# Kernel optimization log

Measured on AMD Instinct MI355X. Metric: run time of the kernel, lower is better.

Reference implementation:

```python
import math
import jax, jax.numpy as jnp
import numpy as np

B, NH, T, N, D = 4, 8, 2048, 256, 512
THETA = 2 ** 16
LN_EPS = 1e-5
RETRIEVAL_SCALE = 1.0
TWO_PI = 2.0 * math.pi


def _freqs(n):
    # get_freqs: 1/theta**(floor(i/2)*2 / n) / (2*pi)
    i = jnp.arange(n, dtype=jnp.float32)
    q = jnp.floor(i / 2.0) * 2.0
    return 1.0 / (THETA ** (q / n)) / TWO_PI


def _rope(phases, v):
    # phases: [1,1,T,N]; v: [B,nh,T,N]
    ph = (phases % 1.0) * TWO_PI
    pc, ps = jnp.cos(ph), jnp.sin(ph)
    ve, vo = v[..., ::2], v[..., 1::2]
    v_rot = jnp.stack((-vo, ve), axis=-1).reshape(v.shape)  # interleaved rotate
    return v * pc + v_rot * ps


def _l2norm(x):
    return x / jnp.maximum(jnp.linalg.norm(x, axis=-1, keepdims=True), 1e-12)


def setup_inputs() -> dict:
    key = jax.random.key(0)
    ks = jax.random.split(key, 8)
    return {
        "Q": jax.random.normal(ks[0], (B, NH, T, N), jnp.float32),
        "V": jax.random.normal(ks[1], (B, NH, T, D), jnp.float32),
        "x_raw": jax.random.normal(ks[2], (B, T, D), jnp.float32),
        "x_next": jax.random.normal(ks[3], (B, T, D), jnp.float32),
        "theta_Q_w": 0.02 * jax.random.normal(ks[4], (N, D), jnp.float32),
        "theta_K_w": 0.02 * jax.random.normal(ks[5], (N, D), jnp.float32),
        "beta_w": 0.02 * jax.random.normal(ks[6], (NH, D), jnp.float32),
        "memory_gate": jnp.full((1, NH, 1, 1), -2.0, jnp.float32),
        "M0": 0.02 * jax.random.normal(ks[7], (B, NH, N, D), jnp.float32),
    }


def _forward(Q, V, x_raw, x_next, theta_Q_w, theta_K_w, beta_w, memory_gate, M0):
    Bq, nh, Tq, Nq = Q.shape
    # ---- causal RoPE linear attention (K is Q; strictly lower-triangular, no softmax)
    freqs = _freqs(Nq)  # [N]
    phases = jnp.arange(Tq, dtype=jnp.float32)[None, None, :, None] * freqs[None, None, None, :]
    QR = _rope(phases, Q)
    scores = jnp.einsum('bhtn,bhsn->bhts', QR, QR)
    mask = jnp.tril(jnp.ones((Tq, Tq), bool), -1)  # diagonal=-1
    scores = jnp.where(mask, scores, 0.0)
    y_standard = scores @ V  # [B,nh,T,D]

    # ---- memory retrieval (position-invariant query)
    Qm = _l2norm(x_raw @ theta_Q_w.T)  # [B,T,N], shared across heads
    y_memory = jnp.einsum('btn,bhnd->bhtd', Qm, M0)
    mu = y_memory.mean(-1, keepdims=True)
    var = y_memory.var(-1, keepdims=True)  # biased, like torch LayerNorm
    y_memory = (y_memory - mu) * jax.lax.rsqrt(var + LN_EPS) * RETRIEVAL_SCALE

    # ---- delta-rule memory update (detached in the original)
    Km = _l2norm(jax.lax.stop_gradient(x_raw @ theta_K_w.T))         # [B,T,N]
    beta = jax.nn.sigmoid(jax.lax.stop_gradient(x_raw @ beta_w.T))   # [B,T,nh]
    Vm = jax.lax.stop_gradient(x_next)                               # [B,T,D]
    M_init = jax.lax.stop_gradient(M0)

    def step(M, inp):
        k, v, b = inp  # k:[B,N] shared across heads, v:[B,D], b:[B,nh]
        v_old = jnp.einsum('bn,bhnd->bhd', k, M)
        v_new = b[..., None] * v[:, None, :] + (1.0 - b[..., None]) * v_old
        M = M + jnp.einsum('bn,bhd->bhnd', k, v_new - v_old)
        return M, None

    M_new, _ = jax.lax.scan(
        step, M_init,
        (jnp.swapaxes(Km, 0, 1), jnp.swapaxes(Vm, 0, 1), jnp.swapaxes(beta, 0, 1)))

    gate = jax.nn.sigmoid(memory_gate)  # [1,nh,1,1]
    y = (1.0 - gate) * y_standard + gate * y_memory
    return y, M_new


def reference(Q, V, x_raw, x_next, theta_Q_w, theta_K_w, beta_w, memory_gate, M0):
    return _forward(Q, V, x_raw, x_next, theta_Q_w, theta_K_w, beta_w, memory_gate, M0)
```

## Files before the change

kernel.cpp:

```cpp
#include <hip/hip_runtime.h>
#include <hip/hip_bf16.h>
#include <math.h>

#define BBATCH 4
#define NHEAD  8
#define TSEQ   2048
#define NDIM   256
#define DDIM   512

typedef float f32x4 __attribute__((ext_vector_type(4)));
typedef short bf16x8 __attribute__((ext_vector_type(8)));

typedef __attribute__((address_space(3))) unsigned int lds_uint;
typedef __attribute__((address_space(1))) unsigned int g_uint;

__device__ __forceinline__ unsigned short f2bf(float f) {
  __hip_bfloat16 h = __float2bfloat16(f);
  return *reinterpret_cast<unsigned short*>(&h);
}
__device__ __forceinline__ float bf2f(unsigned short u) {
  __hip_bfloat16 h;
  *reinterpret_cast<unsigned short*>(&h) = u;
  return __bfloat162float(h);
}
__device__ __forceinline__ f32x4 mfma16(bf16x8 a, bf16x8 b, f32x4 c) {
  return __builtin_amdgcn_mfma_f32_16x16x32_bf16(a, b, c, 0, 0, 0);
}

#define KSW(t) (((((t) & 7) ^ (((t) >> 3) & 3))) << 4)

__global__ __launch_bounds__(256) void rope_kernel(const float* __restrict__ Q,
                                                   unsigned short* __restrict__ QR) {
  long idx = (long)blockIdx.x * 256 + threadIdx.x;
  int pair = (int)(idx & 127);
  long row = idx >> 7;
  int t = (int)(row & (TSEQ - 1));
  float2 q = reinterpret_cast<const float2*>(Q)[idx];
  float freq = exp2f(-(float)pair * 0.125f) * 0.15915494309189535f;
  float phase = (float)t * freq;
  float ph = (phase - floorf(phase)) * 6.283185307179586f;
  float s, c;
  sincosf(ph, &s, &c);
  float o0 = q.x * c - q.y * s;
  float o1 = q.y * c + q.x * s;
  unsigned int pk = (unsigned int)f2bf(o0) | ((unsigned int)f2bf(o1) << 16);
  reinterpret_cast<unsigned int*>(QR)[idx] = pk;
}

__global__ __launch_bounds__(256) void transpose_cast_kernel(
    const float* __restrict__ in, unsigned short* __restrict__ out, int R, int C) {
  __shared__ float tile[64][65];
  long mat = blockIdx.z;
  const float* src = in + mat * (long)R * C;
  unsigned short* dst = out + mat * (long)R * C;
  int c0 = blockIdx.x * 64, r0 = blockIdx.y * 64;
  int tr = threadIdx.x >> 4;
  int tc = (threadIdx.x & 15) * 4;
#pragma unroll
  for (int p = 0; p < 4; ++p) {
    int r = tr + p * 16;
    float4 v = *reinterpret_cast<const float4*>(&src[(long)(r0 + r) * C + c0 + tc]);
    tile[r][tc + 0] = v.x; tile[r][tc + 1] = v.y;
    tile[r][tc + 2] = v.z; tile[r][tc + 3] = v.w;
  }
  __syncthreads();
#pragma unroll
  for (int p = 0; p < 4; ++p) {
    int c = tr + p * 16;
    ushort4 o;
    o.x = f2bf(tile[tc + 0][c]);
    o.y = f2bf(tile[tc + 1][c]);
    o.z = f2bf(tile[tc + 2][c]);
    o.w = f2bf(tile[tc + 3][c]);
    *reinterpret_cast<ushort4*>(&dst[(long)(c0 + c) * R + r0 + tc]) = o;
  }
}

__global__ __launch_bounds__(512) void qkm_kernel(
    const float* __restrict__ x,
    const float* __restrict__ wq,
    const float* __restrict__ wk,
    unsigned short* __restrict__ Qm,
    float* __restrict__ Km) {
  const bool isK = (blockIdx.y == 1);
  const float* w = isK ? wk : wq;
  int r0 = blockIdx.x * 64;
  int wave = threadIdx.x >> 6, lane = threadIdx.x & 63;
  int wm = wave >> 2, wn = wave & 3;
  int khi = lane >> 4, l16 = lane & 15;
  __shared__ unsigned short Ahi[64 * 32], Alo[64 * 32];
  __shared__ unsigned short Bhi[256 * 32], Blo[256 * 32];
  __shared__ float red[4][64];
  f32x4 acc[2][4] = {};
  for (int k0 = 0; k0 < 512; k0 += 32) {
    {
      int row = threadIdx.x >> 3;
      int kc = (threadIdx.x & 7) * 4;
      float4 v = *reinterpret_cast<const float4*>(&x[(long)(r0 + row) * 512 + k0 + kc]);
      float vv[4] = {v.x, v.y, v.z, v.w};
      unsigned int hx[2], lx[2];
      unsigned short h0 = f2bf(vv[0]), h1 = f2bf(vv[1]), h2 = f2bf(vv[2]), h3 = f2bf(vv[3]);
      hx[0] = (unsigned)h0 | ((unsigned)h1 << 16);
      hx[1] = (unsigned)h2 | ((unsigned)h3 << 16);
      lx[0] = (unsigned)f2bf(vv[0] - bf2f(h0)) | ((unsigned)f2bf(vv[1] - bf2f(h1)) << 16);
      lx[1] = (unsigned)f2bf(vv[2] - bf2f(h2)) | ((unsigned)f2bf(vv[3] - bf2f(h3)) << 16);
      int byt = row * 64 + ((kc * 2) ^ ((row & 3) << 4));
      *reinterpret_cast<uint2*>((char*)Ahi + byt) = make_uint2(hx[0], hx[1]);
      *reinterpret_cast<uint2*>((char*)Alo + byt) = make_uint2(lx[0], lx[1]);
    }
#pragma unroll
    for (int p = 0; p < 4; ++p) {
      int idx2 = threadIdx.x + p * 512;
      int row = idx2 >> 3;
      int kc = (idx2 & 7) * 4;
      float4 v = *reinterpret_cast<const float4*>(&w[(long)row * 512 + k0 + kc]);
      float vv[4] = {v.x, v.y, v.z, v.w};
      unsigned short h0 = f2bf(vv[0]), h1 = f2bf(vv[1]), h2 = f2bf(vv[2]), h3 = f2bf(vv[3]);
      unsigned int hx0 = (unsigned)h0 | ((unsigned)h1 << 16);
      unsigned int hx1 = (unsigned)h2 | ((unsigned)h3 << 16);
      unsigned int lx0 = (unsigned)f2bf(vv[0] - bf2f(h0)) | ((unsigned)f2bf(vv[1] - bf2f(h1)) << 16);
      unsigned int lx1 = (unsigned)f2bf(vv[2] - bf2f(h2)) | ((unsigned)f2bf(vv[3] - bf2f(h3)) << 16);
      int byt = row * 64 + ((kc * 2) ^ ((row & 3) << 4));
      *reinterpret_cast<uint2*>((char*)Bhi + byt) = make_uint2(hx0, hx1);
      *reinterpret_cast<uint2*>((char*)Blo + byt) = make_uint2(lx0, lx1);
    }
    __syncthreads();
    bf16x8 ah[2], al[2], bh[4], bl[4];
#pragma unroll
    for (int mi = 0; mi < 2; ++mi) {
      int row = wm * 32 + mi * 16 + l16;
      int byt = row * 64 + ((khi * 16) ^ ((row & 3) << 4));
      ah[mi] = *reinterpret_cast<const bf16x8*>((const char*)Ahi + byt);
      al[mi] = *reinterpret_cast<const bf16x8*>((const char*)Alo + byt);
    }
#pragma unroll
    for (int ni = 0; ni < 4; ++ni) {
      int row = wn * 64 + ni * 16 + l16;
      int byt = row * 64 + ((khi * 16) ^ ((row & 3) << 4));
      bh[ni] = *reinterpret_cast<const bf16x8*>((const char*)Bhi + byt);
      bl[ni] = *reinterpret_cast<const bf16x8*>((const char*)Blo + byt);
    }
#pragma unroll
    for (int mi = 0; mi < 2; ++mi)
#pragma unroll
      for (int ni = 0; ni < 4; ++ni) {
        acc[mi][ni] = mfma16(ah[mi], bh[ni], acc[mi][ni]);
        acc[mi][ni] = mfma16(ah[mi], bl[ni], acc[mi][ni]);
        acc[mi][ni] = mfma16(al[mi], bh[ni], acc[mi][ni]);
      }
    __syncthreads();
  }
  float part[2][4];
#pragma unroll
  for (int mi = 0; mi < 2; ++mi)
#pragma unroll
    for (int r = 0; r < 4; ++r) {
      float s = 0.f;
#pragma unroll
      for (int ni = 0; ni < 4; ++ni) s += acc[mi][ni][r] * acc[mi][ni][r];
      part[mi][r] = s;
    }
#pragma unroll
  for (int off = 1; off < 16; off <<= 1)
#pragma unroll
    for (int mi = 0; mi < 2; ++mi)
#pragma unroll
      for (int r = 0; r < 4; ++r) part[mi][r] += __shfl_xor(part[mi][r], off);
  if (l16 == 0) {
#pragma unroll
    for (int mi = 0; mi < 2; ++mi)
#pragma unroll
      for (int r = 0; r < 4; ++r)
        red[wn][wm * 32 + mi * 16 + khi * 4 + r] = part[mi][r];
  }
  __syncthreads();
#pragma unroll
  for (int mi = 0; mi < 2; ++mi)
#pragma unroll
    for (int r = 0; r < 4; ++r) {
      int row = wm * 32 + mi * 16 + khi * 4 + r;
      float ss = red[0][row] + red[1][row] + red[2][row] + red[3][row];
      float scale = 1.f / fmaxf(sqrtf(ss), 1e-12f);
#pragma unroll
      for (int ni = 0; ni < 4; ++ni) {
        int col = wn * 64 + ni * 16 + l16;
        float val = acc[mi][ni][r] * scale;
        if (isK) Km[(long)(r0 + row) * 256 + col] = val;
        else     Qm[(long)(r0 + row) * 256 + col] = f2bf(val);
      }
    }
}

__global__ __launch_bounds__(64) void beta_kernel(const float* __restrict__ x,
                                                  const float* __restrict__ bw,
                                                  float* __restrict__ beta) {
  long row = blockIdx.x;
  int lane = threadIdx.x;
  const float* xr = x + row * 512;
  float xv[8];
#pragma unroll
  for (int j = 0; j < 8; ++j) xv[j] = xr[lane + j * 64];
#pragma unroll
  for (int hh = 0; hh < 8; ++hh) {
    const float* wr = bw + hh * 512;
    float p = 0.f;
#pragma unroll
    for (int j = 0; j < 8; ++j) p += xv[j] * wr[lane + j * 64];
#pragma unroll
    for (int off = 32; off > 0; off >>= 1) p += __shfl_down(p, off);
    if (lane == 0) beta[row * 8 + hh] = 1.f / (1.f + expf(-p));
  }
}

__global__ __launch_bounds__(256) void wprep_kernel(
    const float* __restrict__ Km, const float* __restrict__ beta,
    unsigned short* __restrict__ Whi, unsigned short* __restrict__ Wlo) {
  __shared__ unsigned short Khi[64 * 256];
  __shared__ unsigned short Klo[64 * 256];
  __shared__ float Bm[64 * 64];
  __shared__ float X[64 * 64];
  __shared__ float bv[64];
  int blk = blockIdx.x, ch = blk & 31, bh = blk >> 5;
  int b = bh >> 3, h = bh & 7;
  int t0 = ch * 64;
  int tid = threadIdx.x, wave = tid >> 6, lane = tid & 63;
  int khi = lane >> 4, l16 = lane & 15;
  {
    int t = tid >> 2, n0 = (tid & 3) * 64;
    const float* kp = Km + ((long)(b * TSEQ) + t0 + t) * 256 + n0;
    char* ph = (char*)Khi + t * 512;
    char* pl = (char*)Klo + t * 512;
#pragma unroll
    for (int i = 0; i < 64; i += 8) {
      float4 v0 = *(const float4*)(kp + i);
      float4 v1 = *(const float4*)(kp + i + 4);
      float vv[8] = {v0.x, v0.y, v0.z, v0.w, v1.x, v1.y, v1.z, v1.w};
      unsigned int hw[4], lw[4];
#pragma unroll
      for (int q = 0; q < 4; ++q) {
        unsigned short h0 = f2bf(vv[2 * q]), h1 = f2bf(vv[2 * q + 1]);
        hw[q] = (unsigned)h0 | ((unsigned)h1 << 16);
        lw[q] = (unsigned)f2bf(vv[2 * q] - bf2f(h0)) |
                ((unsigned)f2bf(vv[2 * q + 1] - bf2f(h1)) << 16);
      }
      int off = ((n0 + i) * 2) ^ ((t & 7) << 4);
      *(uint4*)(ph + off) = make_uint4(hw[0], hw[1], hw[2], hw[3]);
      *(uint4*)(pl + off) = make_uint4(lw[0], lw[1], lw[2], lw[3]);
    }
  }
  if (tid < 64) bv[tid] = beta[((long)(b * TSEQ) + t0 + tid) * 8 + h];
  __syncthreads();
  f32x4 sacc[4] = {};
#pragma unroll
  for (int ks = 0; ks < 8; ++ks) {
    int arow = wave * 16 + l16;
    int koff = (ks * 32 + khi * 8) * 2;
    bf16x8 ah = *(const bf16x8*)((const char*)Khi + arow * 512 + (koff ^ ((arow & 7) << 4)));
    bf16x8 al = *(const bf16x8*)((const char*)Klo + arow * 512 + (koff ^ ((arow & 7) << 4)));
    bf16x8 bhf[4], blf[4];
#pragma unroll
    for (int si = 0; si < 4; ++si) {
      int brow = si * 16 + l16;
      bhf[si] = *(const bf16x8*)((const char*)Khi + brow * 512 + (koff ^ ((brow & 7) << 4)));
      blf[si] = *(const bf16x8*)((const char*)Klo + brow * 512 + (koff ^ ((brow & 7) << 4)));
    }
#pragma unroll
    for (int si = 0; si < 4; ++si) sacc[si] = mfma16(ah, bhf[si], sacc[si]);
#pragma unroll
    for (int si = 0; si < 4; ++si) sacc[si] = mfma16(ah, blf[si], sacc[si]);
#pragma unroll
    for (int si = 0; si < 4; ++si) sacc[si] = mfma16(al, bhf[si], sacc[si]);
  }
#pragma unroll
  for (int si = 0; si < 4; ++si)
#pragma unroll
    for (int r = 0; r < 4; ++r) {
      int t = wave * 16 + khi * 4 + r, s = si * 16 + l16;
      Bm[t * 64 + s] = (s < t) ? bv[t] * sacc[si][r] : 0.f;
    }
  __syncthreads();
  if (wave == 0) {
    for (int t = 0; t < 64; ++t) {
      float xv = (lane == t) ? 1.f : 0.f;
      for (int r = 0; r < t; ++r)
        xv = fmaf(-Bm[t * 64 + r], X[r * 64 + lane], xv);
      X[t * 64 + lane] = xv;
    }
  }
  __syncthreads();
  long base = (long)blk * 4096;
  for (int i = tid; i < 4096; i += 256) {
    int s = i & 63;
    float wv = X[i] * bv[s];
    unsigned short hi = f2bf(wv);
    Whi[base + i] = hi;
    Wlo[base + i] = f2bf(wv - bf2f(hi));
  }
}

__global__ __launch_bounds__(256) void cscan_kernel(
    const float* __restrict__ Km, const float* __restrict__ xn,
    const float* __restrict__ M0,
    const unsigned short* __restrict__ Whi, const unsigned short* __restrict__ Wlo,
    float* __restrict__ Mout) {
  __shared__ unsigned short Mthi[64 * 256];
  __shared__ unsigned short Mtlo[64 * 256];
  __shared__ unsigned short Kr[64 * 256];
  __shared__ unsigned short Wh[64 * 64];
  __shared__ unsigned short Wl[64 * 64];
  __shared__ unsigned short RU0[64 * 64];
  __shared__ unsigned short RU1[64 * 64];
  int blk = blockIdx.x, dsl = blk & 7, bh = blk >> 3;
  int b = bh >> 3;
  int d0 = dsl * 64;
  int tid = threadIdx.x, wave = tid >> 6, lane = tid & 63;
  int khi = lane >> 4, l16 = lane & 15;

  f32x4 macc[4][4];
  const float* M0p = M0 + (long)bh * 256 * 512;
#pragma unroll
  for (int ni = 0; ni < 4; ++ni)
#pragma unroll
    for (int di = 0; di < 4; ++di)
#pragma unroll
      for (int r = 0; r < 4; ++r) {
        int n = wave * 64 + ni * 16 + khi * 4 + r;
        macc[ni][di][r] = M0p[(long)n * 512 + d0 + di * 16 + l16];
      }

#pragma unroll
  for (int ni = 0; ni < 4; ++ni)
#pragma unroll
    for (int di = 0; di < 4; ++di) {
      int n = wave * 64 + ni * 16 + khi * 4;
      int d = di * 16 + l16;
      unsigned short hq[4], lq[4];
#pragma unroll
      for (int r = 0; r < 4; ++r) {
        float v = macc[ni][di][r];
        hq[r] = f2bf(v); lq[r] = f2bf(v - bf2f(hq[r]));
      }
      int off = d * 512 + (((n * 2) ^ ((d & 7) << 4)));
      *(uint2*)((char*)Mthi + off) =
          make_uint2((unsigned)hq[0] | ((unsigned)hq[1] << 16),
                     (unsigned)hq[2] | ((unsigned)hq[3] << 16));
      *(uint2*)((char*)Mtlo + off) =
          make_uint2((unsigned)lq[0] | ((unsigned)lq[1] << 16),
                     (unsigned)lq[2] | ((unsigned)lq[3] << 16));
    }
  __syncthreads();

  for (int ch = 0; ch < 32; ++ch) {
    int tc0 = ch * 64;
    {
      int t = tid >> 2, n0q = (tid & 3) * 64;
      const float* kp = Km + ((long)(b * TSEQ) + tc0 + t) * 256 + n0q;
      char* ph = (char*)Kr + t * 512;
#pragma unroll
      for (int i = 0; i < 64; i += 8) {
        float4 v0 = *(const float4*)(kp + i);
        float4 v1 = *(const float4*)(kp + i + 4);
        unsigned int hw[4];
        hw[0] = (unsigned)f2bf(v0.x) | ((unsigned)f2bf(v0.y) << 16);
        hw[1] = (unsigned)f2bf(v0.z) | ((unsigned)f2bf(v0.w) << 16);
        hw[2] = (unsigned)f2bf(v1.x) | ((unsigned)f2bf(v1.y) << 16);
        hw[3] = (unsigned)f2bf(v1.z) | ((unsigned)f2bf(v1.w) << 16);
        int off = ((n0q + i) * 2) ^ KSW(t);
        *(uint4*)(ph + off) = make_uint4(hw[0], hw[1], hw[2], hw[3]);
      }
    }
    {
      long wbase = ((long)bh * 32 + ch) * 4096;
      int i = tid * 16;
      int t = i >> 6, s = i & 63;
      int o1 = t * 128 + (((s * 2) ^ ((t & 7) << 4)));
      int o2 = t * 128 + ((((s + 8) * 2) ^ ((t & 7) << 4)));
      *(uint4*)((char*)Wh + o1) = *(const uint4*)(Whi + wbase + i);
      *(uint4*)((char*)Wh + o2) = *(const uint4*)(Whi + wbase + i + 8);
      *(uint4*)((char*)Wl + o1) = *(const uint4*)(Wlo + wbase + i);
      *(uint4*)((char*)Wl + o2) = *(const uint4*)(Wlo + wbase + i + 8);
    }
    float vreg[4][4];
    {
      const float* vp = xn + ((long)b * TSEQ + tc0) * 512 + d0;
#pragma unroll
      for (int di = 0; di < 4; ++di)
#pragma unroll
        for (int r = 0; r < 4; ++r) {
          int t = wave * 16 + khi * 4 + r;
          vreg[di][r] = vp[(long)t * 512 + di * 16 + l16];
        }
    }
    __syncthreads();

    f32x4 aacc[4] = {};
#pragma unroll
    for (int ks = 0; ks < 8; ++ks) {
      int arow = wave * 16 + l16;
      int koff = (ks * 32 + khi * 8) * 2;
      bf16x8 af = *(const bf16x8*)((const char*)Kr + arow * 512 + (koff ^ KSW(arow)));
      bf16x8 mh[4], ml[4];
#pragma unroll
      for (int di = 0; di < 4; ++di) {
        int drow = di * 16 + l16;
        mh[di] = *(const bf16x8*)((const char*)Mthi + drow * 512 + (koff ^ ((drow & 7) << 4)));
        ml[di] = *(const bf16x8*)((const char*)Mtlo + drow * 512 + (koff ^ ((drow & 7) << 4)));
      }
#pragma unroll
      for (int di = 0; di < 4; ++di) aacc[di] = mfma16(af, mh[di], aacc[di]);
#pragma unroll
      for (int di = 0; di < 4; ++di) aacc[di] = mfma16(af, ml[di], aacc[di]);
    }
#pragma unroll
    for (int di = 0; di < 4; ++di) {
      int t = wave * 16 + khi * 4;
      int d = di * 16 + l16;
      unsigned short rq[4];
#pragma unroll
      for (int r = 0; r < 4; ++r) rq[r] = f2bf(vreg[di][r] - aacc[di][r]);
      int off = d * 128 + (((t * 2) ^ ((d & 7) << 4)));
      *(uint2*)((char*)RU0 + off) =
          make_uint2((unsigned)rq[0] | ((unsigned)rq[1] << 16),
                     (unsigned)rq[2] | ((unsigned)rq[3] << 16));
    }
    __syncthreads();

    f32x4 uacc[4] = {};
#pragma unroll
    for (int ks = 0; ks < 2; ++ks) {
      int arow = wave * 16 + l16;
      int soff = (ks * 32 + khi * 8) * 2;
      bf16x8 wh_ = *(const bf16x8*)((const char*)Wh + arow * 128 + (soff ^ ((arow & 7) << 4)));
      bf16x8 wl_ = *(const bf16x8*)((const char*)Wl + arow * 128 + (soff ^ ((arow & 7) << 4)));
      bf16x8 rf[4];
#pragma unroll
      for (int di = 0; di < 4; ++di) {
        int drow = di * 16 + l16;
        rf[di] = *(const bf16x8*)((const char*)RU0 + drow * 128 + (soff ^ ((drow & 7) << 4)));
      }
#pragma unroll
      for (int di = 0; di < 4; ++di) uacc[di] = mfma16(wh_, rf[di], uacc[di]);
#pragma unroll
      for (int di = 0; di < 4; ++di) uacc[di] = mfma16(wl_, rf[di], uacc[di]);
    }
    __syncthreads();

#pragma unroll
    for (int di = 0; di < 4; ++di) {
      int t = wave * 16 + khi * 4;
      int d = di * 16 + l16;
      unsigned short hq[4], lq[4];
#pragma unroll
      for (int r = 0; r < 4; ++r) {
        float u = uacc[di][r];
        hq[r] = f2bf(u); lq[r] = f2bf(u - bf2f(hq[r]));
      }
      int off = d * 128 + (((t * 2) ^ ((d & 7) << 4)));
      *(uint2*)((char*)RU0 + off) =
          make_uint2((unsigned)hq[0] | ((unsigned)hq[1] << 16),
                     (unsigned)hq[2] | ((unsigned)hq[3] << 16));
      *(uint2*)((char*)RU1 + off) =
          make_uint2((unsigned)lq[0] | ((unsigned)lq[1] << 16),
                     (unsigned)lq[2] | ((unsigned)lq[3] << 16));
    }
    __syncthreads();

#pragma unroll
    for (int ks = 0; ks < 2; ++ks) {
      bf16x8 ka[4];
#pragma unroll
      for (int ni = 0; ni < 4; ++ni) {
        int n = wave * 64 + ni * 16 + l16;
        bf16x8 kv;
#pragma unroll
        for (int j = 0; j < 8; ++j) {
          int t = ks * 32 + khi * 8 + j;
          kv[j] = *(const short*)((const char*)Kr + t * 512 + (((n * 2) ^ KSW(t))));
        }
        ka[ni] = kv;
      }
      bf16x8 uh[4], ul[4];
#pragma unroll
      for (int di = 0; di < 4; ++di) {
        int drow = di * 16 + l16;
        int toff = (ks * 32 + khi * 8) * 2;
        uh[di] = *(const bf16x8*)((const char*)RU0 + drow * 128 + (toff ^ ((drow & 7) << 4)));
        ul[di] = *(const bf16x8*)((const char*)RU1 + drow * 128 + (toff ^ ((drow & 7) << 4)));
      }
#pragma unroll
      for (int ni = 0; ni < 4; ++ni)
#pragma unroll
        for (int di = 0; di < 4; ++di)
          macc[ni][di] = mfma16(ka[ni], uh[di], macc[ni][di]);
#pragma unroll
      for (int ni = 0; ni < 4; ++ni)
#pragma unroll
        for (int di = 0; di < 4; ++di)
          macc[ni][di] = mfma16(ka[ni], ul[di], macc[ni][di]);
    }
    __syncthreads();

#pragma unroll
    for (int ni = 0; ni < 4; ++ni)
#pragma unroll
      for (int di = 0; di < 4; ++di) {
        int n = wave * 64 + ni * 16 + khi * 4;
        int d = di * 16 + l16;
        unsigned short hq[4], lq[4];
#pragma unroll
        for (int r = 0; r < 4; ++r) {
          float v = macc[ni][di][r];
          hq[r] = f2bf(v); lq[r] = f2bf(v - bf2f(hq[r]));
        }
        int off = d * 512 + (((n * 2) ^ ((d & 7) << 4)));
        *(uint2*)((char*)Mthi + off) =
            make_uint2((unsigned)hq[0] | ((unsigned)hq[1] << 16),
                       (unsigned)hq[2] | ((unsigned)hq[3] << 16));
        *(uint2*)((char*)Mtlo + off) =
            make_uint2((unsigned)lq[0] | ((unsigned)lq[1] << 16),
                       (unsigned)lq[2] | ((unsigned)lq[3] << 16));
      }
    __syncthreads();
  }

  float* Mo = Mout + (long)bh * 256 * 512;
#pragma unroll
  for (int ni = 0; ni < 4; ++ni)
#pragma unroll
    for (int di = 0; di < 4; ++di)
#pragma unroll
      for (int r = 0; r < 4; ++r) {
        int n = wave * 64 + ni * 16 + khi * 4 + r;
        Mo[(long)n * 512 + d0 + di * 16 + l16] = macc[ni][di][r];
      }
}

__global__ __launch_bounds__(512) void attn_kernel(
    const unsigned short* __restrict__ QR,
    const unsigned short* __restrict__ Vt,
    float* __restrict__ Y) {
  int bp = blockIdx.x;
  int bh = blockIdx.y;
  int dch = blockIdx.z;
  int wave = threadIdx.x >> 6, lane = threadIdx.x & 63;
  int wr = wave >> 2, wc = wave & 3;
  int khi = lane >> 4, l16 = lane & 15;
  __shared__ unsigned short K_lds[64 * 256];
  __shared__ unsigned short S_lds[128 * 64];
  const unsigned short* QRb = QR + (long)bh * TSEQ * 256;
  const unsigned short* Vtb = Vt + (long)bh * 512 * TSEQ;
  int d0 = dch * 256;
  float* yb = Y + (long)bh * TSEQ * 512;

  int lin_base = wave * 4096 + lane * 16;

#pragma unroll 1
  for (int half = 0; half < 2; ++half) {
    int bt = half ? bp : (15 - bp);
    int t0 = bt * 128;
    int nst = 2 * bt + 2;

    bf16x8 qa[8];
    {
      int trow = t0 + wave * 16 + l16;
      const unsigned short* qp = QRb + (long)trow * 256 + khi * 8;
#pragma unroll
      for (int ks = 0; ks < 8; ++ks) qa[ks] = *(const bf16x8*)(qp + ks * 32);
    }
    f32x4 acc[4][4] = {};

#pragma unroll
    for (int q = 0; q < 4; ++q) {
      int linear = lin_base + q * 1024;
      int row = linear >> 9;
      int nc2 = (linear & 511) ^ ((row & 7) << 4);
      __builtin_amdgcn_global_load_lds(
          (const g_uint*)((const char*)QRb + (long)row * 512 + nc2),
          (lds_uint*)((char*)K_lds + (wave * 4 + q) * 1024), 16, 0, 0);
    }
    __syncthreads();

    for (int st = 0; st < nst; ++st) {
      int s0 = st * 64;
      f32x4 sacc[4] = {};
#pragma unroll
      for (int ks = 0; ks < 8; ++ks) {
#pragma unroll
        for (int fc = 0; fc < 4; ++fc) {
          int srow = fc * 16 + l16;
          bf16x8 kf = *(const bf16x8*)(
              (const char*)K_lds + srow * 512 + ((ks * 64 + khi * 16) ^ ((srow & 7) << 4)));
          sacc[fc] = mfma16(qa[ks], kf, sacc[fc]);
        }
      }
#pragma unroll
      for (int fc = 0; fc < 4; ++fc)
#pragma unroll
        for (int r = 0; r < 4; ++r) {
          int srow = wave * 16 + khi * 4 + r;
          int scol = fc * 16 + l16;
          float v = ((s0 + scol) < (t0 + srow)) ? sacc[fc][r] : 0.f;
          *(unsigned short*)(
              (char*)S_lds + srow * 128 + ((scol * 2) ^ ((srow & 7) << 4))) = f2bf(v);
        }
      __syncthreads();

      if (st + 1 < nst) {
        long srow_base = (long)(s0 + 64) * 512;
#pragma unroll
        for (int q = 0; q < 4; ++q) {
          int linear = lin_base + q * 1024;
          int row = linear >> 9;
          int nc2 = (linear & 511) ^ ((row & 7) << 4);
          __builtin_amdgcn_global_load_lds(
              (const g_uint*)((const char*)QRb + srow_base + (long)row * 512 + nc2),
              (lds_uint*)((char*)K_lds + (wave * 4 + q) * 1024), 16, 0, 0);
        }
      }
#pragma unroll
      for (int k2 = 0; k2 < 2; ++k2) {
        bf16x8 af[4], bfv[4];
#pragma unroll
        for (int mi = 0; mi < 4; ++mi) {
          int row = wr * 64 + mi * 16 + l16;
          af[mi] = *(const bf16x8*)(
              (const char*)S_lds + row * 128 + ((k2 * 64 + khi * 16) ^ ((row & 7) << 4)));
        }
#pragma unroll
        for (int ni = 0; ni < 4; ++ni) {
          int d = d0 + wc * 64 + ni * 16 + l16;
          bfv[ni] = *(const bf16x8*)(Vtb + (long)d * TSEQ + s0 + k2 * 32 + khi * 8);
        }
#pragma unroll
        for (int mi = 0; mi < 4; ++mi)
#pragma unroll
          for (int ni = 0; ni < 4; ++ni)
            acc[mi][ni] = mfma16(af[mi], bfv[ni], acc[mi][ni]);
      }
      __syncthreads();
    }

#pragma unroll
    for (int mi = 0; mi < 4; ++mi)
#pragma unroll
      for (int ni = 0; ni < 4; ++ni)
#pragma unroll
        for (int r = 0; r < 4; ++r) {
          int trow = t0 + wr * 64 + mi * 16 + khi * 4 + r;
          int d = d0 + wc * 64 + ni * 16 + l16;
          yb[(long)trow * 512 + d] = acc[mi][ni][r];
        }
  }
}

__global__ __launch_bounds__(512) void combine_kernel(
    const unsigned short* __restrict__ Qm,
    const unsigned short* __restrict__ M0t,
    const float* __restrict__ mg,
    float* __restrict__ Y) {
  int t0 = blockIdx.x * 64;
  int bh = blockIdx.y;
  int b = bh >> 3, h = bh & 7;
  int wv = threadIdx.x >> 6, lane = threadIdx.x & 63;
  int khi = lane >> 4, l16 = lane & 15;
  __shared__ unsigned short A_lds[64 * 256];
  __shared__ float red_s[8][64], red_q[8][64];
  __shared__ float mu_s[64], inv_s[64];
  {
    const unsigned short* src = Qm + ((long)b * TSEQ + t0) * 256;
#pragma unroll
    for (int p = 0; p < 4; ++p) {
      int row = (threadIdx.x >> 5) + p * 16;
      int nc = (threadIdx.x & 31) * 8;
      bf16x8 v = *reinterpret_cast<const bf16x8*>(src + (long)row * 256 + nc);
      *reinterpret_cast<bf16x8*>((char*)A_lds + row * 512 + ((nc * 2) ^ ((row & 7) << 4))) = v;
    }
  }
  __syncthreads();
  f32x4 acc[4][4] = {};
  const unsigned short* Bp = M0t + (long)bh * 512 * 256;
#pragma unroll
  for (int ks = 0; ks < 8; ++ks) {
    bf16x8 a[4], bfr[4];
#pragma unroll
    for (int mi = 0; mi < 4; ++mi) {
      int row = mi * 16 + l16;
      a[mi] = *reinterpret_cast<const bf16x8*>(
          (const char*)A_lds + row * 512 + ((ks * 64 + khi * 16) ^ ((row & 7) << 4)));
    }
#pragma unroll
    for (int ni = 0; ni < 4; ++ni) {
      int d = wv * 64 + ni * 16 + l16;
      bfr[ni] = *reinterpret_cast<const bf16x8*>(Bp + (long)d * 256 + ks * 32 + khi * 8);
    }
#pragma unroll
    for (int mi = 0; mi < 4; ++mi)
#pragma unroll
      for (int ni = 0; ni < 4; ++ni)
        acc[mi][ni] = mfma16(a[mi], bfr[ni], acc[mi][ni]);
  }
  float ps[4][4], pq[4][4];
#pragma unroll
  for (int mi = 0; mi < 4; ++mi)
#pragma unroll
    for (int r = 0; r < 4; ++r) {
      float s = 0.f, q = 0.f;
#pragma unroll
      for (int ni = 0; ni < 4; ++ni) {
        float v = acc[mi][ni][r];
        s += v; q += v * v;
      }
      ps[mi][r] = s; pq[mi][r] = q;
    }
#pragma unroll
  for (int off = 1; off < 16; off <<= 1)
#pragma unroll
    for (int mi = 0; mi < 4; ++mi)
#pragma unroll
      for (int r = 0; r < 4; ++r) {
        ps[mi][r] += __shfl_xor(ps[mi][r], off);
        pq[mi][r] += __shfl_xor(pq[mi][r], off);
      }
  if (l16 == 0) {
#pragma unroll
    for (int mi = 0; mi < 4; ++mi)
#pragma unroll
      for (int r = 0; r < 4; ++r) {
        int row = mi * 16 + khi * 4 + r;
        red_s[wv][row] = ps[mi][r];
        red_q[wv][row] = pq[mi][r];
      }
  }
  __syncthreads();
  if (threadIdx.x < 64) {
    float s = 0.f, q = 0.f;
#pragma unroll
    for (int w2 = 0; w2 < 8; ++w2) { s += red_s[w2][threadIdx.x]; q += red_q[w2][threadIdx.x]; }
    float mu = s / 512.f;
    float var = q / 512.f - mu * mu;
    mu_s[threadIdx.x] = mu;
    inv_s[threadIdx.x] = rsqrtf(var + 1e-5f);
  }
  __syncthreads();
  float gate = 1.f / (1.f + expf(-mg[h]));
  float omg = 1.f - gate;
  float* yb = Y + ((long)bh * TSEQ + t0) * 512;
#pragma unroll
  for (int mi = 0; mi < 4; ++mi)
#pragma unroll
    for (int r = 0; r < 4; ++r) {
      int row = mi * 16 + khi * 4 + r;
      float mu = mu_s[row], inv = inv_s[row];
#pragma unroll
      for (int ni = 0; ni < 4; ++ni) {
        int d = wv * 64 + ni * 16 + l16;
        long off = (long)row * 512 + d;
        float ymv = (acc[mi][ni][r] - mu) * inv;
        yb[off] = omg * yb[off] + gate * ymv;
      }
    }
}

extern "C" void kernel_launch(void* const* d_in, const int* in_sizes, int n_in,
                              void* d_out, int out_size, void* d_ws, size_t ws_size,
                              hipStream_t stream) {
  const float* Q      = (const float*)d_in[0];
  const float* V      = (const float*)d_in[1];
  const float* x_raw  = (const float*)d_in[2];
  const float* x_next = (const float*)d_in[3];
  const float* wq     = (const float*)d_in[4];
  const float* wk     = (const float*)d_in[5];
  const float* bw     = (const float*)d_in[6];
  const float* mg     = (const float*)d_in[7];
  const float* M0     = (const float*)d_in[8];
  float* y = (float*)d_out;
  float* Mout = y + (long)32 * 2048 * 512;

  char* ws = (char*)d_ws;
  unsigned short* QR  = (unsigned short*)(ws);
  unsigned short* Vt  = (unsigned short*)(ws + 33554432);
  unsigned short* M0t = (unsigned short*)(ws + 100663296);
  unsigned short* Qm  = (unsigned short*)(ws + 109051904);
  float*  Km          = (float*)(ws + 113246208);
  float*  beta        = (float*)(ws + 121634816);
  unsigned short* Whi = (unsigned short*)(ws + 33554432);
  unsigned short* Wlo = (unsigned short*)(ws + 41943040);

  qkm_kernel<<<dim3(128, 2), dim3(512), 0, stream>>>(x_raw, wq, wk, Qm, Km);
  beta_kernel<<<dim3(8192), dim3(64), 0, stream>>>(x_raw, bw, beta);
  wprep_kernel<<<dim3(1024), dim3(256), 0, stream>>>(Km, beta, Whi, Wlo);
  cscan_kernel<<<dim3(256), dim3(256), 0, stream>>>(Km, x_next, M0, Whi, Wlo, Mout);
  rope_kernel<<<dim3(32768), dim3(256), 0, stream>>>(Q, QR);
  transpose_cast_kernel<<<dim3(8, 32, 32), dim3(256), 0, stream>>>(V, Vt, 2048, 512);
  transpose_cast_kernel<<<dim3(8, 4, 32), dim3(256), 0, stream>>>(M0, M0t, 256, 512);
  attn_kernel<<<dim3(8, 32, 2), dim3(512), 0, stream>>>(QR, Vt, y);
  combine_kernel<<<dim3(32, 32), dim3(512), 0, stream>>>(Qm, M0t, mg, y);
}
```

Before: 853.2 us.

## Precompute bf16 and transposed K, async-load scan operands, widen attention D tile

qkm now also writes a bf16 copy of Km, and a new transpose kernel produces a transposed bf16 Km. The chunked scan reads these with global_load_lds prefetches instead of converting fp32 K and gathering transposed elements one at a time, and it drops one barrier. wprep's triangular solve keeps X in registers and writes W directly, removing the shared X buffer and a second pass. The attention kernel now covers all 512 D columns per block instead of splitting D across two blocks, so S is computed once per tile at the cost of more accumulator registers. These changes add an extra kernel launch and workspace, and the aliased LDS pool and the barrier removal carry race risk.

```diff
diff --git a/kernel.cpp b/kernel.cpp
--- a/kernel.cpp
+++ b/kernel.cpp
@@ -81,7 +81,8 @@
     const float* __restrict__ wq,
     const float* __restrict__ wk,
     unsigned short* __restrict__ Qm,
-    float* __restrict__ Km) {
+    float* __restrict__ Km,
+    unsigned short* __restrict__ Kmb) {
   const bool isK = (blockIdx.y == 1);
   const float* w = isK ? wk : wq;
   int r0 = blockIdx.x * 64;
@@ -185,8 +186,12 @@
       for (int ni = 0; ni < 4; ++ni) {
         int col = wn * 64 + ni * 16 + l16;
         float val = acc[mi][ni][r] * scale;
-        if (isK) Km[(long)(r0 + row) * 256 + col] = val;
-        else     Qm[(long)(r0 + row) * 256 + col] = f2bf(val);
+        if (isK) {
+          Km[(long)(r0 + row) * 256 + col] = val;
+          Kmb[(long)(r0 + row) * 256 + col] = f2bf(val);
+        } else {
+          Qm[(long)(r0 + row) * 256 + col] = f2bf(val);
+        }
       }
     }
 }
@@ -218,7 +223,6 @@
   __shared__ unsigned short Khi[64 * 256];
   __shared__ unsigned short Klo[64 * 256];
   __shared__ float Bm[64 * 64];
-  __shared__ float X[64 * 64];
   __shared__ float bv[64];
   int blk = blockIdx.x, ch = blk & 31, bh = blk >> 5;
   int b = bh >> 3, h = bh & 7;
@@ -280,41 +284,56 @@
     }
   __syncthreads();
   if (wave == 0) {
+    float x[64];
+#pragma unroll
+    for (int i = 0; i < 64; ++i) x[i] = 0.f;
+    long base = (long)blk * 4096;
+    const f32x4* BmV = (const f32x4*)Bm;
+    float bl = bv[lane];
+#pragma unroll
     for (int t = 0; t < 64; ++t) {
-      float xv = (lane == t) ? 1.f : 0.f;
-      for (int r = 0; r < t; ++r)
-        xv = fmaf(-Bm[t * 64 + r], X[r * 64 + lane], xv);
-      X[t * 64 + lane] = xv;
-    }
-  }
-  __syncthreads();
-  long base = (long)blk * 4096;
-  for (int i = tid; i < 4096; i += 256) {
-    int s = i & 63;
-    float wv = X[i] * bv[s];
-    unsigned short hi = f2bf(wv);
-    Whi[base + i] = hi;
-    Wlo[base + i] = f2bf(wv - bf2f(hi));
+      float p0 = 0.f, p1 = 0.f, p2 = 0.f, p3 = 0.f;
+#pragma unroll
+      for (int rq = 0; rq < 16; ++rq) {
+        f32x4 b4 = BmV[t * 16 + rq];
+        p0 = fmaf(b4.x, x[rq * 4 + 0], p0);
+        p1 = fmaf(b4.y, x[rq * 4 + 1], p1);
+        p2 = fmaf(b4.z, x[rq * 4 + 2], p2);
+        p3 = fmaf(b4.w, x[rq * 4 + 3], p3);
+      }
+      float xv = ((lane == t) ? 1.f : 0.f) - ((p0 + p1) + (p2 + p3));
+      x[t] = xv;
+      float wv = xv * bl;
+      unsigned short hi = f2bf(wv);
+      Whi[base + t * 64 + lane] = hi;
+      Wlo[base + t * 64 + lane] = f2bf(wv - bf2f(hi));
+    }
   }
 }
 
 __global__ __launch_bounds__(256) void cscan_kernel(
-    const float* __restrict__ Km, const float* __restrict__ xn,
+    const unsigned short* __restrict__ Kb,
+    const unsigned short* __restrict__ KbT,
+    const float* __restrict__ xn,
     const float* __restrict__ M0,
-    const unsigned short* __restrict__ Whi, const unsigned short* __restrict__ Wlo,
+    const unsigned short* __restrict__ Whi,
+    const unsigned short* __restrict__ Wlo,
     float* __restrict__ Mout) {
   __shared__ unsigned short Mthi[64 * 256];
   __shared__ unsigned short Mtlo[64 * 256];
   __shared__ unsigned short Kr[64 * 256];
-  __shared__ unsigned short Wh[64 * 64];
-  __shared__ unsigned short Wl[64 * 64];
+  __shared__ unsigned short Pool[16384];
   __shared__ unsigned short RU0[64 * 64];
   __shared__ unsigned short RU1[64 * 64];
-  int blk = blockIdx.x, dsl = blk & 7, bh = blk >> 3;
+  unsigned short* Wh = Pool;
+  unsigned short* Wl = Pool + 4096;
+  unsigned short* Krt = Pool;
+  int bh = blockIdx.x, dsl = blockIdx.y;
   int b = bh >> 3;
   int d0 = dsl * 64;
   int tid = threadIdx.x, wave = tid >> 6, lane = tid & 63;
   int khi = lane >> 4, l16 = lane & 15;
+  const char* KbBase = (const char*)(Kb + (long)b * TSEQ * 256);
 
   f32x4 macc[4][4];
   const float* M0p = M0 + (long)bh * 256 * 512;
@@ -327,7 +346,6 @@
         int n = wave * 64 + ni * 16 + khi * 4 + r;
         macc[ni][di][r] = M0p[(long)n * 512 + d0 + di * 16 + l16];
       }
-
 #pragma unroll
   for (int ni = 0; ni < 4; ++ni)
 #pragma unroll
@@ -348,37 +366,31 @@
           make_uint2((unsigned)lq[0] | ((unsigned)lq[1] << 16),
                      (unsigned)lq[2] | ((unsigned)lq[3] << 16));
     }
+#pragma unroll
+  for (int q = 0; q < 8; ++q) {
+    int lin = tid * 16 + q * 4096;
+    int t = lin >> 9;
+    int c = (lin & 511) ^ KSW(t);
+    __builtin_amdgcn_global_load_lds((const g_uint*)(KbBase + (long)t * 512 + c),
+                                     (lds_uint*)((char*)Kr + lin), 16, 0, 0);
+  }
   __syncthreads();
 
   for (int ch = 0; ch < 32; ++ch) {
     int tc0 = ch * 64;
     {
-      int t = tid >> 2, n0q = (tid & 3) * 64;
-      const float* kp = Km + ((long)(b * TSEQ) + tc0 + t) * 256 + n0q;
-      char* ph = (char*)Kr + t * 512;
-#pragma unroll
-      for (int i = 0; i < 64; i += 8) {
-        float4 v0 = *(const float4*)(kp + i);
-        float4 v1 = *(const float4*)(kp + i + 4);
-        unsigned int hw[4];
-        hw[0] = (unsigned)f2bf(v0.x) | ((unsigned)f2bf(v0.y) << 16);
-        hw[1] = (unsigned)f2bf(v0.z) | ((unsigned)f2bf(v0.w) << 16);
-        hw[2] = (unsigned)f2bf(v1.x) | ((unsigned)f2bf(v1.y) << 16);
-        hw[3] = (unsigned)f2bf(v1.z) | ((unsigned)f2bf(v1.w) << 16);
-        int off = ((n0q + i) * 2) ^ KSW(t);
-        *(uint4*)(ph + off) = make_uint4(hw[0], hw[1], hw[2], hw[3]);
-      }
-    }
-    {
-      long wbase = ((long)bh * 32 + ch) * 4096;
-      int i = tid * 16;
-      int t = i >> 6, s = i & 63;
-      int o1 = t * 128 + (((s * 2) ^ ((t & 7) << 4)));
-      int o2 = t * 128 + ((((s + 8) * 2) ^ ((t & 7) << 4)));
-      *(uint4*)((char*)Wh + o1) = *(const uint4*)(Whi + wbase + i);
-      *(uint4*)((char*)Wh + o2) = *(const uint4*)(Whi + wbase + i + 8);
-      *(uint4*)((char*)Wl + o1) = *(const uint4*)(Wlo + wbase + i);
-      *(uint4*)((char*)Wl + o2) = *(const uint4*)(Wlo + wbase + i + 8);
+      const char* whb = (const char*)(Whi + ((long)bh * 32 + ch) * 4096);
+      const char* wlb = (const char*)(Wlo + ((long)bh * 32 + ch) * 4096);
+#pragma unroll
+      for (int q = 0; q < 2; ++q) {
+        int lin = tid * 16 + q * 4096;
+        int t = lin >> 7, c = lin & 127;
+        int sb = t * 128 + (c ^ ((t & 7) << 4));
+        __builtin_amdgcn_global_load_lds((const g_uint*)(whb + sb),
+                                         (lds_uint*)((char*)Wh + lin), 16, 0, 0);
+        __builtin_amdgcn_global_load_lds((const g_uint*)(wlb + sb),
+                                         (lds_uint*)((char*)Wl + lin), 16, 0, 0);
+      }
     }
     float vreg[4][4];
     {
@@ -424,6 +436,18 @@
                      (unsigned)rq[2] | ((unsigned)rq[3] << 16));
     }
     __syncthreads();
+
+    if (ch + 1 < 32) {
+      const char* kb2 = KbBase + (long)(tc0 + 64) * 512;
+#pragma unroll
+      for (int q = 0; q < 8; ++q) {
+        int lin = tid * 16 + q * 4096;
+        int t = lin >> 9;
+        int c = (lin & 511) ^ KSW(t);
+        __builtin_amdgcn_global_load_lds((const g_uint*)(kb2 + (long)t * 512 + c),
+                                         (lds_uint*)((char*)Kr + lin), 16, 0, 0);
+      }
+    }
 
     f32x4 uacc[4] = {};
 #pragma unroll
@@ -445,6 +469,16 @@
     }
     __syncthreads();
 
+    {
+#pragma unroll
+      for (int q = 0; q < 8; ++q) {
+        int lin = tid * 16 + q * 4096;
+        int n = lin >> 7, c = lin & 127;
+        long sb = ((long)(b * 256 + n)) * 4096 + (long)tc0 * 2 + (c ^ ((n & 7) << 4));
+        __builtin_amdgcn_global_load_lds((const g_uint*)((const char*)KbT + sb),
+                                         (lds_uint*)((char*)Krt + lin), 16, 0, 0);
+      }
+    }
 #pragma unroll
     for (int di = 0; di < 4; ++di) {
       int t = wave * 16 + khi * 4;
@@ -467,23 +501,17 @@
 
 #pragma unroll
     for (int ks = 0; ks < 2; ++ks) {
+      int toff = (ks * 32 + khi * 8) * 2;
       bf16x8 ka[4];
 #pragma unroll
       for (int ni = 0; ni < 4; ++ni) {
         int n = wave * 64 + ni * 16 + l16;
-        bf16x8 kv;
-#pragma unroll
-        for (int j = 0; j < 8; ++j) {
-          int t = ks * 32 + khi * 8 + j;
-          kv[j] = *(const short*)((const char*)Kr + t * 512 + (((n * 2) ^ KSW(t))));
-        }
-        ka[ni] = kv;
+        ka[ni] = *(const bf16x8*)((const char*)Krt + n * 128 + (toff ^ ((n & 7) << 4)));
       }
       bf16x8 uh[4], ul[4];
 #pragma unroll
       for (int di = 0; di < 4; ++di) {
         int drow = di * 16 + l16;
-        int toff = (ks * 32 + khi * 8) * 2;
         uh[di] = *(const bf16x8*)((const char*)RU0 + drow * 128 + (toff ^ ((drow & 7) << 4)));
         ul[di] = *(const bf16x8*)((const char*)RU1 + drow * 128 + (toff ^ ((drow & 7) << 4)));
       }
@@ -498,8 +526,6 @@
         for (int di = 0; di < 4; ++di)
           macc[ni][di] = mfma16(ka[ni], ul[di], macc[ni][di]);
     }
-    __syncthreads();
-
 #pragma unroll
     for (int ni = 0; ni < 4; ++ni)
 #pragma unroll
@@ -539,9 +565,8 @@
     const unsigned short* __restrict__ QR,
     const unsigned short* __restrict__ Vt,
     float* __restrict__ Y) {
-  int bp = blockIdx.x;
-  int bh = blockIdx.y;
-  int dch = blockIdx.z;
+  int bh = blockIdx.x;
+  int bp = blockIdx.y;
   int wave = threadIdx.x >> 6, lane = threadIdx.x & 63;
   int wr = wave >> 2, wc = wave & 3;
   int khi = lane >> 4, l16 = lane & 15;
@@ -549,9 +574,7 @@
   __shared__ unsigned short S_lds[128 * 64];
   const unsigned short* QRb = QR + (long)bh * TSEQ * 256;
   const unsigned short* Vtb = Vt + (long)bh * 512 * TSEQ;
-  int d0 = dch * 256;
   float* yb = Y + (long)bh * TSEQ * 512;
-
   int lin_base = wave * 4096 + lane * 16;
 
 #pragma unroll 1
@@ -567,7 +590,7 @@
 #pragma unroll
       for (int ks = 0; ks < 8; ++ks) qa[ks] = *(const bf16x8*)(qp + ks * 32);
     }
-    f32x4 acc[4][4] = {};
+    f32x4 acc[4][8] = {};
 
 #pragma unroll
     for (int q = 0; q < 4; ++q) {
@@ -619,7 +642,7 @@
       }
 #pragma unroll
       for (int k2 = 0; k2 < 2; ++k2) {
-        bf16x8 af[4], bfv[4];
+        bf16x8 af[4];
 #pragma unroll
         for (int mi = 0; mi < 4; ++mi) {
           int row = wr * 64 + mi * 16 + l16;
@@ -627,15 +650,19 @@
               (const char*)S_lds + row * 128 + ((k2 * 64 + khi * 16) ^ ((row & 7) << 4)));
         }
 #pragma unroll
-        for (int ni = 0; ni < 4; ++ni) {
-          int d = d0 + wc * 64 + ni * 16 + l16;
-          bfv[ni] = *(const bf16x8*)(Vtb + (long)d * TSEQ + s0 + k2 * 32 + khi * 8);
+        for (int nh = 0; nh < 2; ++nh) {
+          bf16x8 bfv[4];
+#pragma unroll
+          for (int nj = 0; nj < 4; ++nj) {
+            int d = wc * 128 + (nh * 4 + nj) * 16 + l16;
+            bfv[nj] = *(const bf16x8*)(Vtb + (long)d * TSEQ + s0 + k2 * 32 + khi * 8);
+          }
+#pragma unroll
+          for (int mi = 0; mi < 4; ++mi)
+#pragma unroll
+            for (int nj = 0; nj < 4; ++nj)
+              acc[mi][nh * 4 + nj] = mfma16(af[mi], bfv[nj], acc[mi][nh * 4 + nj]);
         }
-#pragma unroll
-        for (int mi = 0; mi < 4; ++mi)
-#pragma unroll
-          for (int ni = 0; ni < 4; ++ni)
-            acc[mi][ni] = mfma16(af[mi], bfv[ni], acc[mi][ni]);
       }
       __syncthreads();
     }
@@ -643,11 +670,11 @@
 #pragma unroll
     for (int mi = 0; mi < 4; ++mi)
 #pragma unroll
-      for (int ni = 0; ni < 4; ++ni)
+      for (int ni = 0; ni < 8; ++ni)
 #pragma unroll
         for (int r = 0; r < 4; ++r) {
           int trow = t0 + wr * 64 + mi * 16 + khi * 4 + r;
-          int d = d0 + wc * 64 + ni * 16 + l16;
+          int d = wc * 128 + ni * 16 + l16;
           yb[(long)trow * 512 + d] = acc[mi][ni][r];
         }
   }
@@ -785,14 +812,17 @@
   float*  beta        = (float*)(ws + 121634816);
   unsigned short* Whi = (unsigned short*)(ws + 33554432);
   unsigned short* Wlo = (unsigned short*)(ws + 41943040);
-
-  qkm_kernel<<<dim3(128, 2), dim3(512), 0, stream>>>(x_raw, wq, wk, Qm, Km);
+  unsigned short* Kmb = (unsigned short*)(ws + 50331648);
+  unsigned short* KmT = (unsigned short*)(ws + 54525952);
+
+  qkm_kernel<<<dim3(128, 2), dim3(512), 0, stream>>>(x_raw, wq, wk, Qm, Km, Kmb);
+  transpose_cast_kernel<<<dim3(4, 32, 4), dim3(256), 0, stream>>>(Km, KmT, 2048, 256);
   beta_kernel<<<dim3(8192), dim3(64), 0, stream>>>(x_raw, bw, beta);
   wprep_kernel<<<dim3(1024), dim3(256), 0, stream>>>(Km, beta, Whi, Wlo);
-  cscan_kernel<<<dim3(256), dim3(256), 0, stream>>>(Km, x_next, M0, Whi, Wlo, Mout);
+  cscan_kernel<<<dim3(32, 8), dim3(256), 0, stream>>>(Kmb, KmT, x_next, M0, Whi, Wlo, Mout);
   rope_kernel<<<dim3(32768), dim3(256), 0, stream>>>(Q, QR);
   transpose_cast_kernel<<<dim3(8, 32, 32), dim3(256), 0, stream>>>(V, Vt, 2048, 512);
   transpose_cast_kernel<<<dim3(8, 4, 32), dim3(256), 0, stream>>>(M0, M0t, 256, 512);
-  attn_kernel<<<dim3(8, 32, 2), dim3(512), 0, stream>>>(QR, Vt, y);
+  attn_kernel<<<dim3(32, 8), dim3(512), 0, stream>>>(QR, Vt, y);
   combine_kernel<<<dim3(32, 32), dim3(512), 0, stream>>>(Qm, M0t, mg, y);
 }
```

Measured after the change: 708.0 us. 17.0% less time.
